# Optimization experiments

Measured on AMD Instinct MI355X. Metric: run time of the kernel, lower is better.

The kernel has to match this reference:

```python
import jax, jax.numpy as jnp
import numpy as np

B, D_IN, D_BOT, C = 8192, 2048, 1024, 1000
SHARE = 500          # cfg.share_class_num
TEMP = 0.05          # cfg.temp
NEG_FILL = -1e9
EPS = 1e-12          # F.normalize eps


def setup_inputs() -> dict:
    key = jax.random.key(0)
    ks = jax.random.split(key, 6)
    return {
        "features": jax.random.normal(ks[0], (B, D_IN), jnp.float32),
        "W_b": jax.random.normal(ks[1], (D_BOT, D_IN), jnp.float32) * 0.02,
        "b_b": jnp.zeros((D_BOT,), jnp.float32),
        "W1": jax.random.normal(ks[2], (C, D_BOT), jnp.float32) * 0.02,
        "W2": jax.random.normal(ks[3], (C, D_BOT), jnp.float32) * 0.02,
        "centroid": jax.random.normal(ks[4], (C, D_BOT), jnp.float32) * 0.02,
    }


def mask_mechanism(outputs):
    # per-row mask: argmax -> row mask -> masked softmax (branchless)
    predict = jnp.argmax(outputs, axis=1)                       # [B]
    cls = jnp.arange(C)                                          # [C]
    base = cls < SHARE                                           # shared classes masked
    # if predicted class is private (>= SHARE), mask the whole row ...
    row_mask = jnp.where((predict >= SHARE)[:, None], True, base[None, :])
    # ... but always unmask the predicted class itself
    row_mask = row_mask & (cls[None, :] != predict[:, None])     # [B, C] bool
    masked = jnp.where(row_mask, jnp.float32(NEG_FILL), outputs)
    return jax.nn.softmax(masked, axis=1)


def reference(features, W_b, b_b, W1, W2, centroid):
    feats = features @ W_b.T + b_b                               # bottleneck [B, D_BOT]
    outputs1 = feats @ W1.T                                      # [B, C]
    sm1 = mask_mechanism(outputs1)
    feat_oa = sm1 @ centroid                                     # [B, D_BOT]
    features_aug = feats + feat_oa
    # F.normalize(dim=1): x / max(||x||_2, eps)
    norm = jnp.sqrt(jnp.sum(features_aug * features_aug, axis=1, keepdims=True))
    x = features_aug / jnp.maximum(norm, EPS)
    outputs2 = (x @ W2.T) / TEMP                                 # [B, C]
    softmax_outputs = jax.nn.softmax(outputs2, axis=1)
    return (feats, features_aug, outputs1, outputs2, softmax_outputs)
```

## Files before the change

### kernel.cpp

```cpp
#include <hip/hip_runtime.h>
#include <cmath>


typedef _Float16 h8 __attribute__((ext_vector_type(8)));
typedef _Float16 h4 __attribute__((ext_vector_type(4)));
typedef float f32x4 __attribute__((ext_vector_type(4)));

#define TAU 0.015f
#define CAP 1024

__device__ __forceinline__ void gload_lds16(const _Float16* g, _Float16* l) {
    __builtin_amdgcn_global_load_lds(
        (const __attribute__((address_space(1))) void*)g,
        (__attribute__((address_space(3))) void*)l, 16, 0, 0);
}

__global__ void zero_cnt_kernel(int* __restrict__ cnt) { *cnt = 0; }

template <int MODE>
__global__ __launch_bounds__(512, 1) void gemm8p(
    const _Float16* __restrict__ Ah, int lda,
    const _Float16* __restrict__ Bh, int ldb, int K,
    float* __restrict__ C, int ldc, int nC,
    const float* __restrict__ aux, _Float16* __restrict__ Ch)
{
    __shared__ _Float16 sA[3][256 * 64];
    __shared__ _Float16 sB[3][128 * 64];

    const int t = threadIdx.x;
    const int lane = t & 63, wid = t >> 6;
    const int wg = blockIdx.x;
    const int wgid = (wg & 7) * 32 + (wg >> 3);
    const int row0 = (wgid >> 3) * 256, col0 = (wgid & 7) * 128;
    const int wr = wid >> 2, wc = wid & 3;
    const int fr = lane & 15;
    const int fk = (lane >> 4) * 8;
    const int srow = lane >> 3;
    const int scol = (lane & 7) * 8;

    f32x4 acc[8][2] = {};

    auto stage = [&](int b, int kt, int ph) {
        const int kk = kt * 64;
        if (ph == 0 || ph == 1) {
            #pragma unroll
            for (int j = 0; j < 2; ++j) {
                const int i = wid * 4 + ph * 2 + j;
                const int r = i * 8 + srow;
                gload_lds16(Ah + (size_t)(row0 + r) * lda + kk + scol, &sA[b][i * 512]);
            }
        } else if (ph == 2) {
            #pragma unroll
            for (int j = 0; j < 2; ++j) {
                const int i = wid * 2 + j;
                const int r = i * 8 + srow;
                gload_lds16(Bh + (size_t)(col0 + r) * ldb + kk + scol, &sB[b][i * 512]);
            }
        }
    };

    const int NT = K >> 6;
    #pragma unroll
    for (int ph = 0; ph < 3; ++ph) stage(0, 0, ph);
    #pragma unroll
    for (int ph = 0; ph < 3; ++ph) stage(1, 1, ph);
    asm volatile("s_waitcnt vmcnt(6)" ::: "memory");
    __builtin_amdgcn_s_barrier();

    for (int kt = 0; kt < NT; ++kt) {
        const int cb = kt % 3;
        const int pb = (kt + 2) % 3;
        const bool pf = (kt + 2) < NT;
        h8 b0, b1;
        #pragma unroll
        for (int ph = 0; ph < 4; ++ph) {
            const int ks = ph >> 1, mh = ph & 1;
            if (mh == 0) {
                b0 = *(const h8*)&sB[cb][(wc * 32 + fr) * 64 + ks * 32 + fk];
                b1 = *(const h8*)&sB[cb][(wc * 32 + 16 + fr) * 64 + ks * 32 + fk];
            }
            h8 af[4];
            #pragma unroll
            for (int i = 0; i < 4; ++i)
                af[i] = *(const h8*)&sA[cb][(wr * 128 + (mh * 4 + i) * 16 + fr) * 64 + ks * 32 + fk];
            if (pf) stage(pb, kt + 2, ph);
            if (ph == 3) {
                if (pf)             asm volatile("s_waitcnt vmcnt(6)" ::: "memory");
                else if (kt + 1 < NT) asm volatile("s_waitcnt vmcnt(0)" ::: "memory");
            }
            __builtin_amdgcn_s_barrier();
            asm volatile("s_waitcnt lgkmcnt(0)" ::: "memory");
            __builtin_amdgcn_s_setprio(1);
            #pragma unroll
            for (int i = 0; i < 4; ++i) {
                acc[mh * 4 + i][0] = __builtin_amdgcn_mfma_f32_16x16x32_f16(af[i], b0, acc[mh * 4 + i][0], 0, 0, 0);
                acc[mh * 4 + i][1] = __builtin_amdgcn_mfma_f32_16x16x32_f16(af[i], b1, acc[mh * 4 + i][1], 0, 0, 0);
            }
            __builtin_amdgcn_s_setprio(0);
            __builtin_amdgcn_s_barrier();
        }
    }

    #pragma unroll
    for (int mf = 0; mf < 8; ++mf) {
        #pragma unroll
        for (int nf = 0; nf < 2; ++nf) {
            f32x4 v = acc[mf][nf];
            const int gcol = col0 + wc * 32 + nf * 16 + fr;
            const int rbase = row0 + wr * 128 + mf * 16 + (lane >> 4) * 4;
            #pragma unroll
            for (int j = 0; j < 4; ++j) {
                const int grow = rbase + j;
                float val = v[j];
                if constexpr (MODE == 1) val += aux[gcol];
                if constexpr (MODE == 3) val += aux[(size_t)grow * 1024 + gcol];
                if constexpr (MODE == 4) val *= 20.0f;
                if (gcol < nC) {
                    C[(size_t)grow * ldc + gcol] = val;
                    if constexpr (MODE == 1)
                        Ch[(size_t)grow * 1024 + gcol] = (_Float16)val;
                }
            }
        }
    }
}

__global__ __launch_bounds__(256, 2) void gemmc(
    const _Float16* __restrict__ Ah, const _Float16* __restrict__ Al, int lda,
    const _Float16* __restrict__ Bh, const _Float16* __restrict__ Bl, int ldb,
    int klen,
    float* __restrict__ C, int ldc, int nC,
    const int* __restrict__ cnt)
{
    __shared__ _Float16 sAh[128 * 64];
    __shared__ _Float16 sBh[128 * 64];
    __shared__ _Float16 sAl[128 * 64];
    __shared__ _Float16 sBl[128 * 64];

    const int t = threadIdx.x;
    const int lane = t & 63, wid = t >> 6;
    const int row0 = blockIdx.y * 128, col0 = blockIdx.x * 128;
    const int kbase = blockIdx.z * klen;
    if (row0 >= *cnt) return;
    const int wr = wid >> 1, wc = wid & 1;
    const int fr = lane & 15;
    const int fk = (lane >> 4) * 8;
    const int srow = lane >> 3;
    const int scol = (lane & 7) * 8;

    f32x4 acc[4][4] = {};
    f32x4 accc[4][4] = {};

    for (int k0 = kbase; k0 < kbase + klen; k0 += 64) {
        #pragma unroll
        for (int j = 0; j < 4; ++j) {
            int i = wid * 4 + j;
            int r = i * 8 + srow;
            const size_t ga = (size_t)(row0 + r) * lda + k0 + scol;
            const size_t gb = (size_t)(col0 + r) * ldb + k0 + scol;
            gload_lds16(Ah + ga, &sAh[i * 512]);
            gload_lds16(Bh + gb, &sBh[i * 512]);
            gload_lds16(Al + ga, &sAl[i * 512]);
            gload_lds16(Bl + gb, &sBl[i * 512]);
        }
        __syncthreads();
        #pragma unroll
        for (int ks = 0; ks < 2; ++ks) {
            h8 ah[4], al[4];
            #pragma unroll
            for (int mf = 0; mf < 4; ++mf) {
                int rr = wr * 64 + mf * 16 + fr;
                ah[mf] = *(const h8*)&sAh[rr * 64 + ks * 32 + fk];
                al[mf] = *(const h8*)&sAl[rr * 64 + ks * 32 + fk];
            }
            #pragma unroll
            for (int nf = 0; nf < 4; ++nf) {
                int cc = wc * 64 + nf * 16 + fr;
                h8 bh = *(const h8*)&sBh[cc * 64 + ks * 32 + fk];
                h8 bl = *(const h8*)&sBl[cc * 64 + ks * 32 + fk];
                #pragma unroll
                for (int mf = 0; mf < 4; ++mf) {
                    acc[mf][nf]  = __builtin_amdgcn_mfma_f32_16x16x32_f16(ah[mf], bh, acc[mf][nf], 0, 0, 0);
                    accc[mf][nf] = __builtin_amdgcn_mfma_f32_16x16x32_f16(ah[mf], bl, accc[mf][nf], 0, 0, 0);
                    accc[mf][nf] = __builtin_amdgcn_mfma_f32_16x16x32_f16(al[mf], bh, accc[mf][nf], 0, 0, 0);
                }
            }
        }
        __syncthreads();
    }
    float* Cz = C + (size_t)blockIdx.z * CAP * ldc;
    #pragma unroll
    for (int mf = 0; mf < 4; ++mf) {
        #pragma unroll
        for (int nf = 0; nf < 4; ++nf) {
            f32x4 v = acc[mf][nf] + accc[mf][nf] * (1.0f / 2048.0f);
            const int gcol = col0 + wc * 64 + nf * 16 + fr;
            const int rbase = row0 + wr * 64 + mf * 16 + (lane >> 4) * 4;
            #pragma unroll
            for (int j = 0; j < 4; ++j) {
                if (gcol < nC) Cz[(size_t)(rbase + j) * ldc + gcol] = v[j];
            }
        }
    }
}

__global__ void conv_kernel(const float* __restrict__ src, _Float16* __restrict__ hi, int n4)
{
    for (int i = blockIdx.x * 256 + threadIdx.x; i < n4; i += gridDim.x * 256) {
        f32x4 v = ((const f32x4*)src)[i];
        h4 h;
        #pragma unroll
        for (int j = 0; j < 4; ++j) h[j] = (_Float16)v[j];
        ((h4*)hi)[i] = h;
    }
}

__global__ void split_kernel(const float* __restrict__ src,
                             _Float16* __restrict__ hi, _Float16* __restrict__ lo, int n4)
{
    for (int i = blockIdx.x * 256 + threadIdx.x; i < n4; i += gridDim.x * 256) {
        f32x4 v = ((const f32x4*)src)[i];
        h4 h, l;
        #pragma unroll
        for (int j = 0; j < 4; ++j) {
            _Float16 hh = (_Float16)v[j];
            h[j] = hh;
            l[j] = (_Float16)((v[j] - (float)hh) * 2048.0f);
        }
        ((h4*)hi)[i] = h;
        ((h4*)lo)[i] = l;
    }
}

template <bool LO>
__global__ void padsplit_kernel(const float* __restrict__ src,
                                _Float16* __restrict__ hi, _Float16* __restrict__ lo, int nrows)
{
    for (int i = blockIdx.x * 256 + threadIdx.x; i < 1024 * 256; i += gridDim.x * 256) {
        int r = i >> 8;
        f32x4 v = {0.f, 0.f, 0.f, 0.f};
        if (r < nrows) v = ((const f32x4*)src)[i];
        h4 h, l;
        #pragma unroll
        for (int j = 0; j < 4; ++j) {
            _Float16 hh = (_Float16)v[j];
            h[j] = hh;
            if constexpr (LO) l[j] = (_Float16)((v[j] - (float)hh) * 2048.0f);
        }
        ((h4*)hi)[i] = h;
        if constexpr (LO) ((h4*)lo)[i] = l;
    }
}

__global__ __launch_bounds__(256) void ctrans_kernel(const float* __restrict__ centroid,
                                                     _Float16* __restrict__ cT)
{
    __shared__ float tile[32][33];
    const int t = threadIdx.x;
    const int tx = t & 31, ty = t >> 5;
    const int k0 = blockIdx.y * 32, n0 = blockIdx.x * 32;
    #pragma unroll
    for (int p = 0; p < 4; ++p) {
        int k = k0 + ty + p * 8;
        tile[ty + p * 8][tx] = (k < 1000) ? centroid[(size_t)k * 1024 + n0 + tx] : 0.0f;
    }
    __syncthreads();
    #pragma unroll
    for (int p = 0; p < 4; ++p) {
        int n = n0 + ty + p * 8;
        cT[(size_t)n * 1024 + k0 + tx] = (_Float16)tile[tx][ty + p * 8];
    }
}

__device__ __forceinline__ void masked_softmax_body(
    const float* __restrict__ x, _Float16* __restrict__ y,
    int t, float* wv, int* wi, bool flag, int* d_idx, int* d_cnt, int rowid)
{
    float bv = -1e30f, sv = -1e30f; int bi = 0;
    for (int c = t; c < 1000; c += 256) {
        float v = x[c];
        if (v > bv) { sv = bv; bv = v; bi = c; }
        else if (v > sv) sv = v;
    }
    #pragma unroll
    for (int off = 32; off > 0; off >>= 1) {
        float ov = __shfl_down(bv, off, 64);
        int   oi = __shfl_down(bi, off, 64);
        float os = __shfl_down(sv, off, 64);
        if (ov > bv || (ov == bv && oi < bi)) {
            sv = fmaxf(bv, os); bv = ov; bi = oi;
        } else {
            sv = fmaxf(sv, fmaxf(ov, os) == ov ? ov : os);
            sv = fmaxf(sv, ov); sv = fmaxf(sv, os);
        }
    }
    __shared__ float svv[4];
    const int lane = t & 63, wid = t >> 6;
    if (lane == 0) { wv[wid] = bv; wi[wid] = bi; svv[wid] = sv; }
    __syncthreads();
    __shared__ float s_m, s_tot; __shared__ int s_p;
    if (t == 0) {
        float mv = wv[0]; int mi = wi[0]; float m2 = svv[0];
        for (int w = 1; w < 4; ++w) {
            if (wv[w] > mv || (wv[w] == mv && wi[w] < mi)) {
                m2 = fmaxf(mv, svv[w]); mv = wv[w]; mi = wi[w];
            } else {
                m2 = fmaxf(m2, fmaxf(wv[w], svv[w]));
            }
        }
        s_p = mi; s_m = mv;
        if (flag && (mv - m2) < TAU) {
            int slot = atomicAdd(d_cnt, 1);
            if (slot < CAP) d_idx[slot] = rowid;
        }
    }
    __syncthreads();
    const int p = s_p; const float m = s_m;
    if (p >= 500) {
        for (int c = t; c < 1024; c += 256) y[c] = (c == p) ? (_Float16)1.0f : (_Float16)0.0f;
    } else {
        float s = 0.f;
        for (int c = t; c < 1000; c += 256)
            if (c == p || c >= 500) s += expf(x[c] - m);
        #pragma unroll
        for (int off = 32; off > 0; off >>= 1) s += __shfl_down(s, off, 64);
        if (lane == 0) wv[wid] = s;
        __syncthreads();
        if (t == 0) s_tot = wv[0] + wv[1] + wv[2] + wv[3];
        __syncthreads();
        const float inv = 1.0f / s_tot;
        for (int c = t; c < 1024; c += 256) {
            float v = 0.f;
            if (c < 1000 && (c == p || c >= 500)) v = expf(x[c] - m) * inv;
            y[c] = (_Float16)v;
        }
    }
}

__global__ __launch_bounds__(256) void masksm_kernel(const float* __restrict__ o1,
                                                     _Float16* __restrict__ sm,
                                                     int* __restrict__ d_idx,
                                                     int* __restrict__ d_cnt)
{
    __shared__ float wv[4]; __shared__ int wi[4];
    const int row = blockIdx.x;
    masked_softmax_body(o1 + (size_t)row * 1000, sm + (size_t)row * 1024,
                        threadIdx.x, wv, wi, true, d_idx, d_cnt, row);
}

__global__ __launch_bounds__(256) void fixup_kernel(const float* __restrict__ P2,
                                                    _Float16* __restrict__ sm,
                                                    const int* __restrict__ d_idx,
                                                    const int* __restrict__ d_cnt)
{
    const int slot = blockIdx.x;
    if (slot >= *d_cnt || slot >= CAP) return;
    const int row = d_idx[slot];
    const int t = threadIdx.x;
    __shared__ float xr[1000];
    for (int c = t; c < 1000; c += 256) {
        const size_t o = (size_t)slot * 1000 + c;
        xr[c] = P2[o] + P2[o + (size_t)CAP * 1000];
    }
    __syncthreads();
    __shared__ float wv[4]; __shared__ int wi[4];
    masked_softmax_body(xr, sm + (size_t)row * 1024,
                        t, wv, wi, false, nullptr, nullptr, 0);
}

__global__ __launch_bounds__(256) void gather_split_kernel(
    const float* __restrict__ features,
    _Float16* __restrict__ fgh, _Float16* __restrict__ fgl,
    const int* __restrict__ d_idx, const int* __restrict__ d_cnt)
{
    const int slot = blockIdx.x;
    if (slot >= *d_cnt || slot >= CAP) return;
    const int row = d_idx[slot];
    const int t = threadIdx.x;
    #pragma unroll
    for (int q = 0; q < 2; ++q) {
        int o = t * 8 + q * 4;
        f32x4 v = *(const f32x4*)(features + (size_t)row * 2048 + o);
        h4 h, l;
        #pragma unroll
        for (int j = 0; j < 4; ++j) {
            _Float16 hh = (_Float16)v[j];
            h[j] = hh;
            l[j] = (_Float16)((v[j] - (float)hh) * 2048.0f);
        }
        *(h4*)(fgh + (size_t)slot * 2048 + o) = h;
        *(h4*)(fgl + (size_t)slot * 2048 + o) = l;
    }
}

__global__ __launch_bounds__(256) void red1_kernel(const float* __restrict__ P1,
                                                   const float* __restrict__ bias,
                                                   _Float16* __restrict__ fgsh,
                                                   _Float16* __restrict__ fgsl,
                                                   const int* __restrict__ d_cnt)
{
    const int slot = blockIdx.x;
    if (slot >= *d_cnt || slot >= CAP) return;
    const int t = threadIdx.x;
    #pragma unroll
    for (int q = 0; q < 4; ++q) {
        const int c = t + q * 256;
        const size_t o = (size_t)slot * 1024 + c;
        float s = P1[o] + P1[o + (size_t)CAP * 1024] + P1[o + (size_t)2 * CAP * 1024]
                + P1[o + (size_t)3 * CAP * 1024] + bias[c];
        _Float16 h = (_Float16)s;
        fgsh[o] = h;
        fgsl[o] = (_Float16)((s - (float)h) * 2048.0f);
    }
}

__global__ __launch_bounds__(256) void rownorm_x_kernel(const float* __restrict__ aug,
                                                        _Float16* __restrict__ xh)
{
    const int row = blockIdx.x; const int t = threadIdx.x;
    f32x4 v = *((const f32x4*)(aug + (size_t)row * 1024) + t);
    float s = v[0]*v[0] + v[1]*v[1] + v[2]*v[2] + v[3]*v[3];
    #pragma unroll
    for (int off = 32; off > 0; off >>= 1) s += __shfl_down(s, off, 64);
    __shared__ float ws4[4]; __shared__ float s_inv;
    const int lane = t & 63, wid = t >> 6;
    if (lane == 0) ws4[wid] = s;
    __syncthreads();
    if (t == 0) {
        float tot = ws4[0] + ws4[1] + ws4[2] + ws4[3];
        s_inv = 1.0f / fmaxf(sqrtf(tot), 1e-12f);
    }
    __syncthreads();
    const float inv = s_inv;
    h4 h;
    #pragma unroll
    for (int j = 0; j < 4; ++j) h[j] = (_Float16)(v[j] * inv);
    *((h4*)(xh + (size_t)row * 1024) + t) = h;
}

__global__ __launch_bounds__(256) void softmax2_kernel(const float* __restrict__ o2,
                                                       float* __restrict__ out)
{
    const int row = blockIdx.x; const int t = threadIdx.x;
    const float* x = o2 + (size_t)row * 1000;
    float* y = out + (size_t)row * 1000;
    float m = -1e30f;
    for (int c = t; c < 1000; c += 256) m = fmaxf(m, x[c]);
    #pragma unroll
    for (int off = 32; off > 0; off >>= 1) m = fmaxf(m, __shfl_down(m, off, 64));
    __shared__ float sm4[4]; __shared__ float s_m, s_s;
    const int lane = t & 63, wid = t >> 6;
    if (lane == 0) sm4[wid] = m;
    __syncthreads();
    if (t == 0) s_m = fmaxf(fmaxf(sm4[0], sm4[1]), fmaxf(sm4[2], sm4[3]));
    __syncthreads();
    m = s_m;
    float s = 0.f;
    for (int c = t; c < 1000; c += 256) s += expf(x[c] - m);
    #pragma unroll
    for (int off = 32; off > 0; off >>= 1) s += __shfl_down(s, off, 64);
    if (lane == 0) sm4[wid] = s;
    __syncthreads();
    if (t == 0) s_s = sm4[0] + sm4[1] + sm4[2] + sm4[3];
    __syncthreads();
    const float inv = 1.0f / s_s;
    for (int c = t; c < 1000; c += 256) y[c] = expf(x[c] - m) * inv;
}

extern "C" void kernel_launch(void* const* d_in, const int* in_sizes, int n_in,
                              void* d_out, int out_size, void* d_ws, size_t ws_size,
                              hipStream_t stream)
{
    const float* features = (const float*)d_in[0];
    const float* W_b      = (const float*)d_in[1];
    const float* b_b      = (const float*)d_in[2];
    const float* W1       = (const float*)d_in[3];
    const float* W2       = (const float*)d_in[4];
    const float* centroid = (const float*)d_in[5];

    char* base = (char*)d_out;
    float* feats = (float*)(base);
    float* aug   = (float*)(base + 33554432);
    float* o1    = (float*)(base + 67108864);
    float* o2    = (float*)(base + 99876864);
    float* smx   = (float*)(base + 132644864);

    _Float16* fh    = (_Float16*)(base + 67108864);
    _Float16* fetsh = (_Float16*)(base + 33554432);
    float*    P1    = (float*)   (base + 33554432);
    float*    P2    = (float*)   (base + 33554432);
    int*      idx   = (int*)     (base + 50331648);
    int*      cnt   = (int*)     (base + 50339840);
    _Float16* fgsh  = (_Float16*)(base + 50348032);
    _Float16* fgsl  = (_Float16*)(base + 52445184);
    _Float16* sm1h  = (_Float16*)(base + 99876864);
    _Float16* cth   = (_Float16*)(base + 116654080);
    _Float16* wbh   = (_Float16*)(base + 118751232);
    _Float16* wbl   = (_Float16*)(base + 122945536);
    _Float16* w2h   = (_Float16*)(base + 132644864);
    _Float16* w1h   = (_Float16*)(base + 142606336);
    _Float16* w1l   = (_Float16*)(base + 144703488);
    _Float16* fgh   = (_Float16*)(base + 146800640);
    _Float16* fgl   = (_Float16*)(base + 150994944);
    _Float16* xh    = (_Float16*)(base + 146800640);

    zero_cnt_kernel<<<1, 1, 0, stream>>>(cnt);

    conv_kernel<<<2048, 256, 0, stream>>>(features, fh, 4194304);
    split_kernel<<<1024, 256, 0, stream>>>(W_b, wbh, wbl, 524288);
    padsplit_kernel<true><<<1024, 256, 0, stream>>>(W1, w1h, w1l, 1000);
    ctrans_kernel<<<dim3(32, 32), 256, 0, stream>>>(centroid, cth);
    padsplit_kernel<false><<<1024, 256, 0, stream>>>(W2, w2h, nullptr, 1000);

    gemm8p<1><<<256, 512, 0, stream>>>(fh, 2048, wbh, 2048, 2048,
                                       feats, 1024, 1024, b_b, fetsh);
    gemm8p<2><<<256, 512, 0, stream>>>(fetsh, 1024, w1h, 1024, 1024,
                                       o1, 1000, 1000, nullptr, nullptr);
    masksm_kernel<<<8192, 256, 0, stream>>>(o1, sm1h, idx, cnt);

    gather_split_kernel<<<CAP, 256, 0, stream>>>(features, fgh, fgl, idx, cnt);
    gemmc<<<dim3(8, CAP / 128, 4), 256, 0, stream>>>(fgh, fgl, 2048, wbh, wbl, 2048, 512,
                                                     P1, 1024, 1024, cnt);
    red1_kernel<<<CAP, 256, 0, stream>>>(P1, b_b, fgsh, fgsl, cnt);
    gemmc<<<dim3(8, CAP / 128, 2), 256, 0, stream>>>(fgsh, fgsl, 1024, w1h, w1l, 1024, 512,
                                                     P2, 1000, 1000, cnt);
    fixup_kernel<<<CAP, 256, 0, stream>>>(P2, sm1h, idx, cnt);

    gemm8p<3><<<256, 512, 0, stream>>>(sm1h, 1024, cth, 1024, 1024,
                                       aug, 1024, 1024, feats, nullptr);
    rownorm_x_kernel<<<8192, 256, 0, stream>>>(aug, xh);
    gemm8p<4><<<256, 512, 0, stream>>>(xh, 1024, w2h, 1024, 1024,
                                       o2, 1000, 1000, nullptr, nullptr);
    softmax2_kernel<<<8192, 256, 0, stream>>>(o2, smx);
}
```

Measured before the change: 311.9 us.

## Fuse prep kernels, merge gather into masked softmax, swap GEMM for simpler 128x128 tile

Five conversion kernels plus the counter reset are merged into one block-range-dispatched prep kernel. The gather/split of near-tie rows now happens inside the masked-softmax kernel, which drops one launch. The triple-buffered 256x128 pipelined GEMM is replaced by a single-buffered 128x128 tile GEMM with 4 blocks per CU. TAU is lowered from 0.015 to 0.010, so fewer rows are flagged for high-precision recompute. That threshold change trades accuracy margin for less work, and the simpler GEMM gives up software pipelining in favour of occupancy.

```diff
diff --git a/kernel.cpp b/kernel.cpp
--- a/kernel.cpp
+++ b/kernel.cpp
@@ -6,7 +6,7 @@
 typedef _Float16 h4 __attribute__((ext_vector_type(4)));
 typedef float f32x4 __attribute__((ext_vector_type(4)));
 
-#define TAU 0.015f
+#define TAU 0.010f
 #define CAP 1024
 
 __device__ __forceinline__ void gload_lds16(const _Float16* g, _Float16* l) {
@@ -15,99 +15,136 @@
         (__attribute__((address_space(3))) void*)l, 16, 0, 0);
 }
 
-__global__ void zero_cnt_kernel(int* __restrict__ cnt) { *cnt = 0; }
+__device__ __forceinline__ void split4(f32x4 v, h4& h, h4& l) {
+    #pragma unroll
+    for (int j = 0; j < 4; ++j) {
+        _Float16 hh = (_Float16)v[j];
+        h[j] = hh;
+        l[j] = (_Float16)((v[j] - (float)hh) * 2048.0f);
+    }
+}
+
+__global__ __launch_bounds__(256) void prep_kernel(
+    const float* __restrict__ features, _Float16* __restrict__ fh,
+    const float* __restrict__ W_b, _Float16* __restrict__ wbh, _Float16* __restrict__ wbl,
+    const float* __restrict__ W1, _Float16* __restrict__ w1h, _Float16* __restrict__ w1l,
+    const float* __restrict__ W2, _Float16* __restrict__ w2h,
+    const float* __restrict__ centroid, _Float16* __restrict__ cth,
+    int* __restrict__ cnt)
+{
+    __shared__ float tile[32][33];
+    const int bid = blockIdx.x;
+    const int t = threadIdx.x;
+    if (bid == 0 && t == 0) *cnt = 0;
+
+    if (bid < 2048) {
+        for (int i = bid * 256 + t; i < 4194304; i += 2048 * 256) {
+            f32x4 v = ((const f32x4*)features)[i];
+            h4 h;
+            #pragma unroll
+            for (int j = 0; j < 4; ++j) h[j] = (_Float16)v[j];
+            ((h4*)fh)[i] = h;
+        }
+    } else if (bid < 3072) {
+        const int i = (bid - 2048) * 512 + t;
+        #pragma unroll
+        for (int q = 0; q < 2; ++q) {
+            const int k = i + q * 256;
+            f32x4 v = ((const f32x4*)W_b)[k];
+            h4 h, l; split4(v, h, l);
+            ((h4*)wbh)[k] = h;
+            ((h4*)wbl)[k] = l;
+        }
+    } else if (bid < 4096) {
+        const int i = (bid - 3072) * 256 + t;
+        const int r = i >> 8;
+        f32x4 v = {0.f, 0.f, 0.f, 0.f};
+        if (r < 1000) v = ((const f32x4*)W1)[i];
+        h4 h, l; split4(v, h, l);
+        ((h4*)w1h)[i] = h;
+        ((h4*)w1l)[i] = l;
+    } else if (bid < 5120) {
+        const int local = bid - 4096;
+        const int n0 = (local & 31) * 32, k0 = (local >> 5) * 32;
+        const int tx = t & 31, ty = t >> 5;
+        #pragma unroll
+        for (int p = 0; p < 4; ++p) {
+            int k = k0 + ty + p * 8;
+            tile[ty + p * 8][tx] = (k < 1000) ? centroid[(size_t)k * 1024 + n0 + tx] : 0.0f;
+        }
+        __syncthreads();
+        #pragma unroll
+        for (int p = 0; p < 4; ++p) {
+            int n = n0 + ty + p * 8;
+            cth[(size_t)n * 1024 + k0 + tx] = (_Float16)tile[tx][ty + p * 8];
+        }
+    } else {
+        const int i = (bid - 5120) * 256 + t;
+        const int r = i >> 8;
+        f32x4 v = {0.f, 0.f, 0.f, 0.f};
+        if (r < 1000) v = ((const f32x4*)W2)[i];
+        h4 h;
+        #pragma unroll
+        for (int j = 0; j < 4; ++j) h[j] = (_Float16)v[j];
+        ((h4*)w2h)[i] = h;
+    }
+}
 
 template <int MODE>
-__global__ __launch_bounds__(512, 1) void gemm8p(
+__global__ __launch_bounds__(256, 4) void gemm16(
     const _Float16* __restrict__ Ah, int lda,
     const _Float16* __restrict__ Bh, int ldb, int K,
     float* __restrict__ C, int ldc, int nC,
     const float* __restrict__ aux, _Float16* __restrict__ Ch)
 {
-    __shared__ _Float16 sA[3][256 * 64];
-    __shared__ _Float16 sB[3][128 * 64];
+    __shared__ _Float16 sAh[128 * 64];
+    __shared__ _Float16 sBh[128 * 64];
 
     const int t = threadIdx.x;
     const int lane = t & 63, wid = t >> 6;
     const int wg = blockIdx.x;
-    const int wgid = (wg & 7) * 32 + (wg >> 3);
-    const int row0 = (wgid >> 3) * 256, col0 = (wgid & 7) * 128;
-    const int wr = wid >> 2, wc = wid & 3;
+    const int wgid = (wg & 7) * 64 + (wg >> 3);
+    const int row0 = (wgid >> 3) * 128, col0 = (wgid & 7) * 128;
+    const int wr = wid >> 1, wc = wid & 1;
     const int fr = lane & 15;
     const int fk = (lane >> 4) * 8;
     const int srow = lane >> 3;
     const int scol = (lane & 7) * 8;
 
-    f32x4 acc[8][2] = {};
-
-    auto stage = [&](int b, int kt, int ph) {
-        const int kk = kt * 64;
-        if (ph == 0 || ph == 1) {
-            #pragma unroll
-            for (int j = 0; j < 2; ++j) {
-                const int i = wid * 4 + ph * 2 + j;
-                const int r = i * 8 + srow;
-                gload_lds16(Ah + (size_t)(row0 + r) * lda + kk + scol, &sA[b][i * 512]);
-            }
-        } else if (ph == 2) {
-            #pragma unroll
-            for (int j = 0; j < 2; ++j) {
-                const int i = wid * 2 + j;
-                const int r = i * 8 + srow;
-                gload_lds16(Bh + (size_t)(col0 + r) * ldb + kk + scol, &sB[b][i * 512]);
-            }
-        }
-    };
-
-    const int NT = K >> 6;
-    #pragma unroll
-    for (int ph = 0; ph < 3; ++ph) stage(0, 0, ph);
-    #pragma unroll
-    for (int ph = 0; ph < 3; ++ph) stage(1, 1, ph);
-    asm volatile("s_waitcnt vmcnt(6)" ::: "memory");
-    __builtin_amdgcn_s_barrier();
-
-    for (int kt = 0; kt < NT; ++kt) {
-        const int cb = kt % 3;
-        const int pb = (kt + 2) % 3;
-        const bool pf = (kt + 2) < NT;
-        h8 b0, b1;
-        #pragma unroll
-        for (int ph = 0; ph < 4; ++ph) {
-            const int ks = ph >> 1, mh = ph & 1;
-            if (mh == 0) {
-                b0 = *(const h8*)&sB[cb][(wc * 32 + fr) * 64 + ks * 32 + fk];
-                b1 = *(const h8*)&sB[cb][(wc * 32 + 16 + fr) * 64 + ks * 32 + fk];
-            }
-            h8 af[4];
-            #pragma unroll
-            for (int i = 0; i < 4; ++i)
-                af[i] = *(const h8*)&sA[cb][(wr * 128 + (mh * 4 + i) * 16 + fr) * 64 + ks * 32 + fk];
-            if (pf) stage(pb, kt + 2, ph);
-            if (ph == 3) {
-                if (pf)             asm volatile("s_waitcnt vmcnt(6)" ::: "memory");
-                else if (kt + 1 < NT) asm volatile("s_waitcnt vmcnt(0)" ::: "memory");
-            }
-            __builtin_amdgcn_s_barrier();
-            asm volatile("s_waitcnt lgkmcnt(0)" ::: "memory");
-            __builtin_amdgcn_s_setprio(1);
-            #pragma unroll
-            for (int i = 0; i < 4; ++i) {
-                acc[mh * 4 + i][0] = __builtin_amdgcn_mfma_f32_16x16x32_f16(af[i], b0, acc[mh * 4 + i][0], 0, 0, 0);
-                acc[mh * 4 + i][1] = __builtin_amdgcn_mfma_f32_16x16x32_f16(af[i], b1, acc[mh * 4 + i][1], 0, 0, 0);
-            }
-            __builtin_amdgcn_s_setprio(0);
-            __builtin_amdgcn_s_barrier();
-        }
-    }
-
-    #pragma unroll
-    for (int mf = 0; mf < 8; ++mf) {
-        #pragma unroll
-        for (int nf = 0; nf < 2; ++nf) {
+    f32x4 acc[4][4] = {};
+
+    for (int k0 = 0; k0 < K; k0 += 64) {
+        #pragma unroll
+        for (int j = 0; j < 4; ++j) {
+            int i = wid * 4 + j;
+            int r = i * 8 + srow;
+            gload_lds16(Ah + (size_t)(row0 + r) * lda + k0 + scol, &sAh[i * 512]);
+            gload_lds16(Bh + (size_t)(col0 + r) * ldb + k0 + scol, &sBh[i * 512]);
+        }
+        __syncthreads();
+        #pragma unroll
+        for (int ks = 0; ks < 2; ++ks) {
+            h8 ah[4];
+            #pragma unroll
+            for (int mf = 0; mf < 4; ++mf)
+                ah[mf] = *(const h8*)&sAh[(wr * 64 + mf * 16 + fr) * 64 + ks * 32 + fk];
+            #pragma unroll
+            for (int nf = 0; nf < 4; ++nf) {
+                h8 bh = *(const h8*)&sBh[(wc * 64 + nf * 16 + fr) * 64 + ks * 32 + fk];
+                #pragma unroll
+                for (int mf = 0; mf < 4; ++mf)
+                    acc[mf][nf] = __builtin_amdgcn_mfma_f32_16x16x32_f16(ah[mf], bh, acc[mf][nf], 0, 0, 0);
+            }
+        }
+        __syncthreads();
+    }
+    #pragma unroll
+    for (int mf = 0; mf < 4; ++mf) {
+        #pragma unroll
+        for (int nf = 0; nf < 4; ++nf) {
             f32x4 v = acc[mf][nf];
-            const int gcol = col0 + wc * 32 + nf * 16 + fr;
-            const int rbase = row0 + wr * 128 + mf * 16 + (lane >> 4) * 4;
+            const int gcol = col0 + wc * 64 + nf * 16 + fr;
+            const int rbase = row0 + wr * 64 + mf * 16 + (lane >> 4) * 4;
             #pragma unroll
             for (int j = 0; j < 4; ++j) {
                 const int grow = rbase + j;
@@ -204,77 +241,10 @@
     }
 }
 
-__global__ void conv_kernel(const float* __restrict__ src, _Float16* __restrict__ hi, int n4)
-{
-    for (int i = blockIdx.x * 256 + threadIdx.x; i < n4; i += gridDim.x * 256) {
-        f32x4 v = ((const f32x4*)src)[i];
-        h4 h;
-        #pragma unroll
-        for (int j = 0; j < 4; ++j) h[j] = (_Float16)v[j];
-        ((h4*)hi)[i] = h;
-    }
-}
-
-__global__ void split_kernel(const float* __restrict__ src,
-                             _Float16* __restrict__ hi, _Float16* __restrict__ lo, int n4)
-{
-    for (int i = blockIdx.x * 256 + threadIdx.x; i < n4; i += gridDim.x * 256) {
-        f32x4 v = ((const f32x4*)src)[i];
-        h4 h, l;
-        #pragma unroll
-        for (int j = 0; j < 4; ++j) {
-            _Float16 hh = (_Float16)v[j];
-            h[j] = hh;
-            l[j] = (_Float16)((v[j] - (float)hh) * 2048.0f);
-        }
-        ((h4*)hi)[i] = h;
-        ((h4*)lo)[i] = l;
-    }
-}
-
-template <bool LO>
-__global__ void padsplit_kernel(const float* __restrict__ src,
-                                _Float16* __restrict__ hi, _Float16* __restrict__ lo, int nrows)
-{
-    for (int i = blockIdx.x * 256 + threadIdx.x; i < 1024 * 256; i += gridDim.x * 256) {
-        int r = i >> 8;
-        f32x4 v = {0.f, 0.f, 0.f, 0.f};
-        if (r < nrows) v = ((const f32x4*)src)[i];
-        h4 h, l;
-        #pragma unroll
-        for (int j = 0; j < 4; ++j) {
-            _Float16 hh = (_Float16)v[j];
-            h[j] = hh;
-            if constexpr (LO) l[j] = (_Float16)((v[j] - (float)hh) * 2048.0f);
-        }
-        ((h4*)hi)[i] = h;
-        if constexpr (LO) ((h4*)lo)[i] = l;
-    }
-}
-
-__global__ __launch_bounds__(256) void ctrans_kernel(const float* __restrict__ centroid,
-                                                     _Float16* __restrict__ cT)
-{
-    __shared__ float tile[32][33];
-    const int t = threadIdx.x;
-    const int tx = t & 31, ty = t >> 5;
-    const int k0 = blockIdx.y * 32, n0 = blockIdx.x * 32;
-    #pragma unroll
-    for (int p = 0; p < 4; ++p) {
-        int k = k0 + ty + p * 8;
-        tile[ty + p * 8][tx] = (k < 1000) ? centroid[(size_t)k * 1024 + n0 + tx] : 0.0f;
-    }
-    __syncthreads();
-    #pragma unroll
-    for (int p = 0; p < 4; ++p) {
-        int n = n0 + ty + p * 8;
-        cT[(size_t)n * 1024 + k0 + tx] = (_Float16)tile[tx][ty + p * 8];
-    }
-}
-
 __device__ __forceinline__ void masked_softmax_body(
     const float* __restrict__ x, _Float16* __restrict__ y,
-    int t, float* wv, int* wi, bool flag, int* d_idx, int* d_cnt, int rowid)
+    int t, float* wv, int* wi, bool flag, int* d_idx, int* d_cnt, int rowid,
+    int* s_slot)
 {
     float bv = -1e30f, sv = -1e30f; int bi = 0;
     for (int c = t; c < 1000; c += 256) {
@@ -309,10 +279,12 @@
             }
         }
         s_p = mi; s_m = mv;
+        int slot = -1;
         if (flag && (mv - m2) < TAU) {
-            int slot = atomicAdd(d_cnt, 1);
-            if (slot < CAP) d_idx[slot] = rowid;
-        }
+            int q = atomicAdd(d_cnt, 1);
+            if (q < CAP) { d_idx[q] = rowid; slot = q; }
+        }
+        *s_slot = slot;
     }
     __syncthreads();
     const int p = s_p; const float m = s_m;
@@ -337,15 +309,28 @@
     }
 }
 
-__global__ __launch_bounds__(256) void masksm_kernel(const float* __restrict__ o1,
-                                                     _Float16* __restrict__ sm,
-                                                     int* __restrict__ d_idx,
-                                                     int* __restrict__ d_cnt)
-{
-    __shared__ float wv[4]; __shared__ int wi[4];
+__global__ __launch_bounds__(256) void masksm_kernel(
+    const float* __restrict__ o1, _Float16* __restrict__ sm,
+    const float* __restrict__ features,
+    _Float16* __restrict__ fgh, _Float16* __restrict__ fgl,
+    int* __restrict__ d_idx, int* __restrict__ d_cnt)
+{
+    __shared__ float wv[4]; __shared__ int wi[4]; __shared__ int s_slot;
     const int row = blockIdx.x;
+    const int t = threadIdx.x;
     masked_softmax_body(o1 + (size_t)row * 1000, sm + (size_t)row * 1024,
-                        threadIdx.x, wv, wi, true, d_idx, d_cnt, row);
+                        t, wv, wi, true, d_idx, d_cnt, row, &s_slot);
+    const int slot = s_slot;
+    if (slot >= 0) {
+        #pragma unroll
+        for (int q = 0; q < 2; ++q) {
+            int o = t * 8 + q * 4;
+            f32x4 v = *(const f32x4*)(features + (size_t)row * 2048 + o);
+            h4 h, l; split4(v, h, l);
+            *(h4*)(fgh + (size_t)slot * 2048 + o) = h;
+            *(h4*)(fgl + (size_t)slot * 2048 + o) = l;
+        }
+    }
 }
 
 __global__ __launch_bounds__(256) void fixup_kernel(const float* __restrict__ P2,
@@ -363,34 +348,9 @@
         xr[c] = P2[o] + P2[o + (size_t)CAP * 1000];
     }
     __syncthreads();
-    __shared__ float wv[4]; __shared__ int wi[4];
+    __shared__ float wv[4]; __shared__ int wi[4]; __shared__ int s_slot;
     masked_softmax_body(xr, sm + (size_t)row * 1024,
-                        t, wv, wi, false, nullptr, nullptr, 0);
-}
-
-__global__ __launch_bounds__(256) void gather_split_kernel(
-    const float* __restrict__ features,
-    _Float16* __restrict__ fgh, _Float16* __restrict__ fgl,
-    const int* __restrict__ d_idx, const int* __restrict__ d_cnt)
-{
-    const int slot = blockIdx.x;
-    if (slot >= *d_cnt || slot >= CAP) return;
-    const int row = d_idx[slot];
-    const int t = threadIdx.x;
-    #pragma unroll
-    for (int q = 0; q < 2; ++q) {
-        int o = t * 8 + q * 4;
-        f32x4 v = *(const f32x4*)(features + (size_t)row * 2048 + o);
-        h4 h, l;
-        #pragma unroll
-        for (int j = 0; j < 4; ++j) {
-            _Float16 hh = (_Float16)v[j];
-            h[j] = hh;
-            l[j] = (_Float16)((v[j] - (float)hh) * 2048.0f);
-        }
-        *(h4*)(fgh + (size_t)slot * 2048 + o) = h;
-        *(h4*)(fgl + (size_t)slot * 2048 + o) = l;
-    }
+                        t, wv, wi, false, nullptr, nullptr, 0, &s_slot);
 }
 
 __global__ __launch_bounds__(256) void red1_kernel(const float* __restrict__ P1,
@@ -504,32 +464,23 @@
     _Float16* fgl   = (_Float16*)(base + 150994944);
     _Float16* xh    = (_Float16*)(base + 146800640);
 
-    zero_cnt_kernel<<<1, 1, 0, stream>>>(cnt);
-
-    conv_kernel<<<2048, 256, 0, stream>>>(features, fh, 4194304);
-    split_kernel<<<1024, 256, 0, stream>>>(W_b, wbh, wbl, 524288);
-    padsplit_kernel<true><<<1024, 256, 0, stream>>>(W1, w1h, w1l, 1000);
-    ctrans_kernel<<<dim3(32, 32), 256, 0, stream>>>(centroid, cth);
-    padsplit_kernel<false><<<1024, 256, 0, stream>>>(W2, w2h, nullptr, 1000);
-
-    gemm8p<1><<<256, 512, 0, stream>>>(fh, 2048, wbh, 2048, 2048,
+    prep_kernel<<<6144, 256, 0, stream>>>(features, fh, W_b, wbh, wbl,
+                                          W1, w1h, w1l, W2, w2h, centroid, cth, cnt);
+    gemm16<1><<<512, 256, 0, stream>>>(fh, 2048, wbh, 2048, 2048,
                                        feats, 1024, 1024, b_b, fetsh);
-    gemm8p<2><<<256, 512, 0, stream>>>(fetsh, 1024, w1h, 1024, 1024,
+    gemm16<2><<<512, 256, 0, stream>>>(fetsh, 1024, w1h, 1024, 1024,
                                        o1, 1000, 1000, nullptr, nullptr);
-    masksm_kernel<<<8192, 256, 0, stream>>>(o1, sm1h, idx, cnt);
-
-    gather_split_kernel<<<CAP, 256, 0, stream>>>(features, fgh, fgl, idx, cnt);
+    masksm_kernel<<<8192, 256, 0, stream>>>(o1, sm1h, features, fgh, fgl, idx, cnt);
     gemmc<<<dim3(8, CAP / 128, 4), 256, 0, stream>>>(fgh, fgl, 2048, wbh, wbl, 2048, 512,
                                                      P1, 1024, 1024, cnt);
     red1_kernel<<<CAP, 256, 0, stream>>>(P1, b_b, fgsh, fgsl, cnt);
     gemmc<<<dim3(8, CAP / 128, 2), 256, 0, stream>>>(fgsh, fgsl, 1024, w1h, w1l, 1024, 512,
                                                      P2, 1000, 1000, cnt);
     fixup_kernel<<<CAP, 256, 0, stream>>>(P2, sm1h, idx, cnt);
-
-    gemm8p<3><<<256, 512, 0, stream>>>(sm1h, 1024, cth, 1024, 1024,
+    gemm16<3><<<512, 256, 0, stream>>>(sm1h, 1024, cth, 1024, 1024,
                                        aug, 1024, 1024, feats, nullptr);
     rownorm_x_kernel<<<8192, 256, 0, stream>>>(aug, xh);
-    gemm8p<4><<<256, 512, 0, stream>>>(xh, 1024, w2h, 1024, 1024,
+    gemm16<4><<<512, 256, 0, stream>>>(xh, 1024, w2h, 1024, 1024,
                                        o2, 1000, 1000, nullptr, nullptr);
     softmax2_kernel<<<8192, 256, 0, stream>>>(o2, smx);
 }
```

After: 288.3 us. -7.6%, faster.
